# Kernel optimization log

Measured on AMD Instinct MI355X. Metric: run time of the kernel, lower is better.

## Reference

```python
import jax, jax.numpy as jnp
import numpy as np

H = 128          # hidden_channels == num_features for both node types
L = 3            # num_layers
E_TYPES = 3      # (a->a), (a->b), (b->a)
N = 200000       # nodes per type
E = 600000       # edges per edge type
G = 64           # graphs in batch
C = 10           # num_classes
BN_EPS = 1e-5


def setup_inputs() -> dict:
    key = jax.random.key(0)
    ks = jax.random.split(key, 16)
    x_a = jax.random.normal(ks[0], (N, H), dtype=jnp.float32)
    x_b = jax.random.normal(ks[1], (N, H), dtype=jnp.float32)
    ei_aa = jax.random.randint(ks[2], (2, E), 0, N, dtype=jnp.int32)
    ei_ab = jax.random.randint(ks[3], (2, E), 0, N, dtype=jnp.int32)
    ei_ba = jax.random.randint(ks[4], (2, E), 0, N, dtype=jnp.int32)
    batch_a = jnp.sort(jax.random.randint(ks[5], (N,), 0, G, dtype=jnp.int32))
    batch_b = jnp.sort(jax.random.randint(ks[6], (N,), 0, G, dtype=jnp.int32))
    s = 1.0 / np.sqrt(H)
    # GraphConv params per (layer, edge_type): lin_rel (weight+bias), lin_root (no bias)
    Wrel = jax.random.uniform(ks[7], (L, E_TYPES, H, H), jnp.float32, -s, s)
    brel = jax.random.uniform(ks[8], (L, E_TYPES, H), jnp.float32, -s, s)
    Wroot = jax.random.uniform(ks[9], (L, E_TYPES, H, H), jnp.float32, -s, s)
    # BatchNorm affine params per node type (0='a', 1='b')
    bn_gamma = jnp.ones((2, H), jnp.float32)
    bn_beta = jnp.zeros((2, H), jnp.float32)
    lin_W = jax.random.uniform(ks[10], (C, H), jnp.float32, -s, s)
    lin_b = jax.random.uniform(ks[11], (C,), jnp.float32, -s, s)
    return {"x_a": x_a, "x_b": x_b, "Wrel": Wrel, "brel": brel, "Wroot": Wroot,
            "bn_gamma": bn_gamma, "bn_beta": bn_beta, "lin_W": lin_W, "lin_b": lin_b,
            "ei_aa": ei_aa, "ei_ab": ei_ab, "ei_ba": ei_ba,
            "batch_a": batch_a, "batch_b": batch_b}


def _graph_conv(x_src, x_dst, ei, W_rel, b_rel, W_root):
    # PyG GraphConv (aggr='add'): out = lin_rel(sum_{j in N(i)} x_j) + lin_root(x_i)
    agg = jax.ops.segment_sum(x_src[ei[0]], ei[1], num_segments=x_dst.shape[0])
    return agg @ W_rel.T + b_rel + x_dst @ W_root.T


def _bn(x, gamma, beta):
    # BatchNorm in training mode: batch statistics (biased variance)
    mu = x.mean(axis=0)
    var = x.var(axis=0)
    return gamma * (x - mu) * jax.lax.rsqrt(var + BN_EPS) + beta


def reference(x_a, x_b, Wrel, brel, Wroot, bn_gamma, bn_beta, lin_W, lin_b,
              ei_aa, ei_ab, ei_ba, batch_a, batch_b):
    for l in range(L):
        # HeteroConv sums contributions per destination node type
        out_a = (_graph_conv(x_a, x_a, ei_aa, Wrel[l, 0], brel[l, 0], Wroot[l, 0]) +
                 _graph_conv(x_b, x_a, ei_ba, Wrel[l, 2], brel[l, 2], Wroot[l, 2]))
        out_b = _graph_conv(x_a, x_b, ei_ab, Wrel[l, 1], brel[l, 1], Wroot[l, 1])
        x_a = _bn(jax.nn.relu(out_a), bn_gamma[0], bn_beta[0])
        x_b = _bn(jax.nn.relu(out_b), bn_gamma[1], bn_beta[1])
    # global mean pool over concatenated node types
    feats = jnp.concatenate([x_a, x_b], axis=0)
    batch = jnp.concatenate([batch_a, batch_b], axis=0)
    sums = jax.ops.segment_sum(feats, batch, num_segments=G)
    counts = jax.ops.segment_sum(jnp.ones((feats.shape[0],), feats.dtype), batch, num_segments=G)
    pooled = sums / jnp.maximum(counts, 1.0)[:, None]
    return pooled @ lin_W.T + lin_b
```

## Files before the change

### kernel.cpp

```cpp
#include <hip/hip_runtime.h>
#include <hip/hip_bf16.h>

#define HF 128

typedef unsigned int uint32;
typedef unsigned short ushort16;
typedef float f32x4 __attribute__((ext_vector_type(4)));
typedef __bf16 bf16x8 __attribute__((ext_vector_type(8)));

__device__ __forceinline__ float bflo(uint32 u) { return __uint_as_float(u << 16); }
__device__ __forceinline__ float bfhi(uint32 u) { return __uint_as_float(u & 0xffff0000u); }
__device__ __forceinline__ ushort16 f2bf(float f) {
  uint32 u = __float_as_uint(f);
  return (ushort16)((u + 0x7fffu + ((u >> 16) & 1u)) >> 16);
}
__device__ __forceinline__ uint32 pack2(float lo, float hi) {
  return (uint32)f2bf(lo) | ((uint32)f2bf(hi) << 16);
}

__global__ void diag_k(float* __restrict__ out, int n, float val) {
  int i = blockIdx.x * 256 + threadIdx.x;
  if (i < n) out[i] = val;
}

__global__ void init_k(float* __restrict__ ss, float* __restrict__ pool, int Gn) {
  int idx = blockIdx.x * 256 + threadIdx.x;
  if (idx < 512) ss[idx] = (idx < 128 || (idx >= 256 && idx < 384)) ? 1.f : 0.f;
  int p = idx - 512;
  if (p >= 0 && p < Gn * HF) pool[p] = 0.f;
}

__global__ void conv_k(const float* __restrict__ in, uint32* __restrict__ out, int n4) {
  int i = blockIdx.x * 256 + threadIdx.x;
  if (i >= n4) return;
  float4 v = ((const float4*)in)[i];
  uint2 p;
  p.x = pack2(v.x, v.y);
  p.y = pack2(v.z, v.w);
  ((uint2*)out)[i] = p;
}

__global__ void count_k(const int* __restrict__ ei, int E, int* __restrict__ rp) {
  int e = blockIdx.x * 256 + threadIdx.x;
  if (e < E) atomicAdd(&rp[ei[E + e]], 1);
}

__global__ __launch_bounds__(256) void scan1_k(const int* __restrict__ rp, int N,
                                               int* __restrict__ bsum) {
  int b = blockIdx.x, t = threadIdx.x;
  int i = b * 1024 + t * 4;
  int s = 0;
  if (i + 3 < N) {
    int4 v = *(const int4*)&rp[i];
    s = v.x + v.y + v.z + v.w;
  } else {
    for (int j = 0; j < 4; ++j) if (i + j < N) s += rp[i + j];
  }
  __shared__ int sd[256];
  sd[t] = s;
  __syncthreads();
  for (int o = 128; o > 0; o >>= 1) {
    if (t < o) sd[t] += sd[t + o];
    __syncthreads();
  }
  if (t == 0) bsum[b] = sd[0];
}

__global__ __launch_bounds__(1024) void scan2_k(int* __restrict__ bsum, int nb) {
  __shared__ int sd[1024];
  int t = threadIdx.x;
  int v = (t < nb) ? bsum[t] : 0;
  sd[t] = v;
  __syncthreads();
  for (int o = 1; o < 1024; o <<= 1) {
    int x = (t >= o) ? sd[t - o] : 0;
    __syncthreads();
    sd[t] += x;
    __syncthreads();
  }
  if (t < nb) bsum[t] = sd[t] - v;
}

__global__ __launch_bounds__(256) void scan3_k(int* __restrict__ rp, int* __restrict__ cur,
                                               const int* __restrict__ bsum, int N) {
  int b = blockIdx.x, t = threadIdx.x;
  int i = b * 1024 + t * 4;
  int c[4];
  #pragma unroll
  for (int j = 0; j < 4; ++j) c[j] = (i + j < N) ? rp[i + j] : 0;
  int tsum = c[0] + c[1] + c[2] + c[3];
  __shared__ int sd[256];
  sd[t] = tsum;
  __syncthreads();
  for (int o = 1; o < 256; o <<= 1) {
    int x = (t >= o) ? sd[t - o] : 0;
    __syncthreads();
    sd[t] += x;
    __syncthreads();
  }
  int off = bsum[b] + sd[t] - tsum;
  int p = off;
  #pragma unroll
  for (int j = 0; j < 4; ++j) {
    if (i + j < N) { rp[i + j] = p; cur[i + j] = p; }
    p += c[j];
  }
  if (i < N && N <= i + 4) rp[N] = off + tsum;
}

__global__ void fill_k(const int* __restrict__ ei, int E, int* __restrict__ cur,
                       int* __restrict__ cs) {
  int e = blockIdx.x * 256 + threadIdx.x;
  if (e >= E) return;
  int dst = ei[E + e];
  int pos = atomicAdd(&cur[dst], 1);
  cs[pos] = ei[e];
}

__global__ __launch_bounds__(128) void prep2_k(
    const float* __restrict__ Wrel_l, const float* __restrict__ Wroot_l,
    const float* __restrict__ brel_l, const float* __restrict__ ss,
    ushort16* __restrict__ BWa, ushort16* __restrict__ BWb,
    float* __restrict__ uvec) {
  __shared__ float red[128];
  int n = blockIdx.x, k = threadIdx.x;
  float scA = ss[k], shA = ss[128 + k], scB = ss[256 + k], shB = ss[384 + k];
  float w0  = Wrel_l[n * HF + k];
  float w1  = Wrel_l[16384 + n * HF + k];
  float w2  = Wrel_l[32768 + n * HF + k];
  float wr1 = Wroot_l[16384 + n * HF + k];
  float wrc = Wroot_l[n * HF + k] + Wroot_l[32768 + n * HF + k];

  int ksl = k >> 5;
  int lane = (n & 15) + (((k >> 3) & 3) << 4);
  int j = k & 7;
  int nt = n >> 4;
  auto put = [&](ushort16* B, int ksb, float v) {
    B[((size_t)((ksb + ksl) * 8 + nt) * 64 + lane) * 8 + j] = f2bf(v);
  };
  put(BWa, 0, scA * w0);
  put(BWa, 4, scB * w2);
  put(BWa, 8, scA * wrc);
  put(BWb, 0, scA * w1);
  put(BWb, 4, scB * wr1);

  auto reduce = [&](float v) -> float {
    red[k] = v;
    __syncthreads();
    for (int s = 64; s > 0; s >>= 1) {
      if (k < s) red[k] += red[k + s];
      __syncthreads();
    }
    float r = red[0];
    __syncthreads();
    return r;
  };
  float r0 = reduce(shA * w0);
  float r1 = reduce(shB * w2);
  float r2 = reduce(shA * w1);
  float r3 = reduce(shA * wrc);
  float r4 = reduce(shB * wr1);
  if (k == 0) {
    uvec[n]       = r0;
    uvec[128 + n] = r1;
    uvec[256 + n] = r2;
    uvec[384 + n] = brel_l[n] + brel_l[256 + n] + r3;
    uvec[512 + n] = brel_l[128 + n] + r4;
  }
}

template <bool HAS2>
__global__ __launch_bounds__(256) void gg_k(
    const uint32* __restrict__ Xg1, const int* __restrict__ rp1, const int* __restrict__ cs1,
    const uint32* __restrict__ Xg2, const int* __restrict__ rp2, const int* __restrict__ cs2,
    const uint32* Xr,
    const bf16x8* __restrict__ BW,
    const float* __restrict__ u1, const float* __restrict__ u2,
    const float* __restrict__ bias,
    uint32* out,
    float* __restrict__ statS, float* __restrict__ statQ,
    int nRows) {
  constexpr int KS_G = HAS2 ? 8 : 4;
  constexpr int WDW = HAS2 ? 2048 : 1088;
  __shared__ uint32 lds[4][WDW];
  int tid = threadIdx.x, wid = tid >> 6, l = tid & 63;
  int R0 = blockIdx.x * 64 + wid * 16;
  uint32* L = &lds[wid][0];
  int grp = l >> 4, sub = l & 15;
  int row = l & 15, khi = l >> 4;

  int grr = R0 + row;
  bf16x8 rt[4];
  #pragma unroll
  for (int ks = 0; ks < 4; ++ks) {
    rt[ks] = bf16x8{};
    if (grr < nRows)
      rt[ks] = *(const bf16x8*)&Xr[(size_t)grr * 64 + ks * 16 + khi * 4];
  }

  #pragma unroll
  for (int rr = 0; rr < 4; ++rr) {
    int r = rr * 4 + grp;
    int gr = R0 + r;
    int dstOff = r * 64 + ((sub ^ (r & 7)) << 2);
    {
      float a0=0.f,a1=0.f,a2=0.f,a3=0.f,a4=0.f,a5=0.f,a6=0.f,a7=0.f;
      if (gr < nRows) {
        int e0 = rp1[gr], e1 = rp1[gr + 1];
        int e = e0;
        for (; e + 2 <= e1; e += 2) {
          int s0 = cs1[e], s1 = cs1[e + 1];
          uint4 v0 = *(const uint4*)&Xg1[(size_t)s0 * 64 + sub * 4];
          uint4 v1 = *(const uint4*)&Xg1[(size_t)s1 * 64 + sub * 4];
          a0 += bflo(v0.x) + bflo(v1.x); a1 += bfhi(v0.x) + bfhi(v1.x);
          a2 += bflo(v0.y) + bflo(v1.y); a3 += bfhi(v0.y) + bfhi(v1.y);
          a4 += bflo(v0.z) + bflo(v1.z); a5 += bfhi(v0.z) + bfhi(v1.z);
          a6 += bflo(v0.w) + bflo(v1.w); a7 += bfhi(v0.w) + bfhi(v1.w);
        }
        if (e < e1) {
          uint4 v = *(const uint4*)&Xg1[(size_t)cs1[e] * 64 + sub * 4];
          a0 += bflo(v.x); a1 += bfhi(v.x); a2 += bflo(v.y); a3 += bfhi(v.y);
          a4 += bflo(v.z); a5 += bfhi(v.z); a6 += bflo(v.w); a7 += bfhi(v.w);
        }
      }
      uint4 p;
      p.x = pack2(a0, a1); p.y = pack2(a2, a3);
      p.z = pack2(a4, a5); p.w = pack2(a6, a7);
      *(uint4*)&L[dstOff] = p;
    }
    if constexpr (HAS2) {
      float a0=0.f,a1=0.f,a2=0.f,a3=0.f,a4=0.f,a5=0.f,a6=0.f,a7=0.f;
      if (gr < nRows) {
        int e0 = rp2[gr], e1 = rp2[gr + 1];
        int e = e0;
        for (; e + 2 <= e1; e += 2) {
          int s0 = cs2[e], s1 = cs2[e + 1];
          uint4 v0 = *(const uint4*)&Xg2[(size_t)s0 * 64 + sub * 4];
          uint4 v1 = *(const uint4*)&Xg2[(size_t)s1 * 64 + sub * 4];
          a0 += bflo(v0.x) + bflo(v1.x); a1 += bfhi(v0.x) + bfhi(v1.x);
          a2 += bflo(v0.y) + bflo(v1.y); a3 += bfhi(v0.y) + bfhi(v1.y);
          a4 += bflo(v0.z) + bflo(v1.z); a5 += bfhi(v0.z) + bfhi(v1.z);
          a6 += bflo(v0.w) + bflo(v1.w); a7 += bfhi(v0.w) + bfhi(v1.w);
        }
        if (e < e1) {
          uint4 v = *(const uint4*)&Xg2[(size_t)cs2[e] * 64 + sub * 4];
          a0 += bflo(v.x); a1 += bfhi(v.x); a2 += bflo(v.y); a3 += bfhi(v.y);
          a4 += bflo(v.z); a5 += bfhi(v.z); a6 += bflo(v.w); a7 += bfhi(v.w);
        }
      }
      uint4 p;
      p.x = pack2(a0, a1); p.y = pack2(a2, a3);
      p.z = pack2(a4, a5); p.w = pack2(a6, a7);
      *(uint4*)&L[1024 + dstOff] = p;
    }
  }

  f32x4 acc[8] = {};
  #pragma unroll
  for (int ks = 0; ks < 4; ++ks) {
    int d = row * 64 + (((ks * 4 + khi) ^ (row & 7)) << 2);
    bf16x8 a = *(const bf16x8*)&L[d];
    const bf16x8* Bp = BW + (size_t)(ks * 8) * 64 + l;
    #pragma unroll
    for (int nt = 0; nt < 8; ++nt) {
      bf16x8 b = Bp[(size_t)nt * 64];
      acc[nt] = __builtin_amdgcn_mfma_f32_16x16x32_bf16(a, b, acc[nt], 0, 0, 0);
    }
  }
  if constexpr (HAS2) {
    #pragma unroll
    for (int ks = 0; ks < 4; ++ks) {
      int d = 1024 + row * 64 + (((ks * 4 + khi) ^ (row & 7)) << 2);
      bf16x8 a = *(const bf16x8*)&L[d];
      const bf16x8* Bp = BW + (size_t)((4 + ks) * 8) * 64 + l;
      #pragma unroll
      for (int nt = 0; nt < 8; ++nt) {
        bf16x8 b = Bp[(size_t)nt * 64];
        acc[nt] = __builtin_amdgcn_mfma_f32_16x16x32_bf16(a, b, acc[nt], 0, 0, 0);
      }
    }
  }
  #pragma unroll
  for (int ks = 0; ks < 4; ++ks) {
    const bf16x8* Bp = BW + (size_t)((KS_G + ks) * 8) * 64 + l;
    #pragma unroll
    for (int nt = 0; nt < 8; ++nt) {
      bf16x8 b = Bp[(size_t)nt * 64];
      acc[nt] = __builtin_amdgcn_mfma_f32_16x16x32_bf16(rt[ks], b, acc[nt], 0, 0, 0);
    }
  }

  int rl0 = khi * 4;
  float deg1v[4], deg2v[4];
  #pragma unroll
  for (int j = 0; j < 4; ++j) {
    int r = R0 + rl0 + j;
    deg1v[j] = (r < nRows) ? (float)(rp1[r + 1] - rp1[r]) : 0.f;
    if constexpr (HAS2) deg2v[j] = (r < nRows) ? (float)(rp2[r + 1] - rp2[r]) : 0.f;
    else deg2v[j] = 0.f;
  }
  ushort16* P = (ushort16*)L;
  int c0 = l & 15;
  float ps[8], pq[8];
  #pragma unroll
  for (int nt = 0; nt < 8; ++nt) {
    int col = nt * 16 + c0;
    float bc = bias[col];
    float u1c = u1[col];
    float u2c = HAS2 ? u2[col] : 0.f;
    float s = 0.f, q = 0.f;
    #pragma unroll
    for (int j = 0; j < 4; ++j) {
      float v = acc[nt][j] + bc + deg1v[j] * u1c;
      if constexpr (HAS2) v += deg2v[j] * u2c;
      v = fmaxf(v, 0.f);
      if (R0 + rl0 + j < nRows) { s += v; q += v * v; }
      P[(rl0 + j) * 136 + col] = f2bf(v);
    }
    ps[nt] = s; pq[nt] = q;
  }

  #pragma unroll
  for (int rr = 0; rr < 4; ++rr) {
    int rloc = rr * 4 + khi;
    int grow = R0 + rloc;
    if (grow < nRows) {
      uint4 v = *(const uint4*)&P[rloc * 136 + c0 * 8];
      *(uint4*)&out[(size_t)grow * 64 + c0 * 4] = v;
    }
  }

  #pragma unroll
  for (int nt = 0; nt < 8; ++nt) {
    ps[nt] += __shfl_xor(ps[nt], 16); ps[nt] += __shfl_xor(ps[nt], 32);
    pq[nt] += __shfl_xor(pq[nt], 16); pq[nt] += __shfl_xor(pq[nt], 32);
  }
  if (l < 16) {
    float* S = statS + (size_t)(blockIdx.x & 63) * 128;
    float* Q = statQ + (size_t)(blockIdx.x & 63) * 128;
    #pragma unroll
    for (int nt = 0; nt < 8; ++nt) {
      unsafeAtomicAdd(&S[nt * 16 + l], ps[nt]);
      unsafeAtomicAdd(&Q[nt * 16 + l], pq[nt]);
    }
  }
}

__global__ void bn_fin_k(const float* __restrict__ stats, const float* __restrict__ gamma,
                         const float* __restrict__ beta, float* __restrict__ ss,
                         float nA, float nB) {
  int t = threadIdx.x;
  if (t >= 256) return;
  int type = t >> 7, f = t & 127;
  const float* S = stats + (size_t)type * 16384;
  const float* Q = S + 8192;
  float s = 0.f, q = 0.f;
  for (int st = 0; st < 64; ++st) { s += S[st * 128 + f]; q += Q[st * 128 + f]; }
  float nN = type ? nB : nA;
  float mean = s / nN;
  float var = q / nN - mean * mean;
  float rstd = rsqrtf(var + 1e-5f);
  float sc = gamma[type * HF + f] * rstd;
  float sh = beta[type * HF + f] - mean * sc;
  ss[type * 256 + f] = sc;
  ss[type * 256 + 128 + f] = sh;
}

__global__ __launch_bounds__(256) void pool_k(const uint32* __restrict__ x,
                                              const int* __restrict__ batch,
                                              const float* __restrict__ scale,
                                              const float* __restrict__ shift,
                                              float* __restrict__ pool, int nN) {
  int f2 = threadIdx.x & 31;
  int sub = threadIdx.x >> 5;
  int start = blockIdx.x * 1024;
  int end = min(start + 1024, nN);
  float4 sc = *(const float4*)&scale[f2 * 4];
  float4 sh = *(const float4*)&shift[f2 * 4];
  float a0 = 0.f, a1 = 0.f, a2 = 0.f, a3 = 0.f, cnt = 0.f;
  int cur = -1;
  for (int n = start + sub; n < end; n += 8) {
    int g = batch[n];
    if (g != cur) {
      if (cur >= 0) {
        float* bp = &pool[(size_t)cur * HF + f2 * 4];
        unsafeAtomicAdd(bp + 0, sc.x * a0 + cnt * sh.x);
        unsafeAtomicAdd(bp + 1, sc.y * a1 + cnt * sh.y);
        unsafeAtomicAdd(bp + 2, sc.z * a2 + cnt * sh.z);
        unsafeAtomicAdd(bp + 3, sc.w * a3 + cnt * sh.w);
      }
      a0 = a1 = a2 = a3 = 0.f; cnt = 0.f; cur = g;
    }
    uint2 v = *(const uint2*)&x[(size_t)n * 64 + f2 * 2];
    a0 += bflo(v.x); a1 += bfhi(v.x); a2 += bflo(v.y); a3 += bfhi(v.y);
    cnt += 1.f;
  }
  if (cur >= 0) {
    float* bp = &pool[(size_t)cur * HF + f2 * 4];
    unsafeAtomicAdd(bp + 0, sc.x * a0 + cnt * sh.x);
    unsafeAtomicAdd(bp + 1, sc.y * a1 + cnt * sh.y);
    unsafeAtomicAdd(bp + 2, sc.z * a2 + cnt * sh.z);
    unsafeAtomicAdd(bp + 3, sc.w * a3 + cnt * sh.w);
  }
}

__device__ inline int lowerb(const int* a, int n, int v) {
  int lo = 0, hi = n;
  while (lo < hi) { int m = (lo + hi) >> 1; if (a[m] < v) lo = m + 1; else hi = m; }
  return lo;
}

__global__ void counts_k(const int* __restrict__ ba, int nA, const int* __restrict__ bb, int nB,
                         float* __restrict__ counts, int Gn) {
  for (int g = threadIdx.x; g < Gn; g += blockDim.x) {
    int c = (lowerb(ba, nA, g + 1) - lowerb(ba, nA, g)) +
            (lowerb(bb, nB, g + 1) - lowerb(bb, nB, g));
    counts[g] = fmaxf((float)c, 1.f);
  }
}

__global__ void final_k(const float* __restrict__ pool, const float* __restrict__ counts,
                        const float* __restrict__ linW, const float* __restrict__ linb,
                        float* __restrict__ out, int Cn) {
  int g = blockIdx.x;
  int lane = threadIdx.x;
  float inv = 1.f / counts[g];
  float p0 = pool[(size_t)g * HF + lane] * inv;
  float p1 = pool[(size_t)g * HF + 64 + lane] * inv;
  for (int c = 0; c < Cn; ++c) {
    float t = p0 * linW[c * HF + lane] + p1 * linW[c * HF + 64 + lane];
    for (int off = 32; off > 0; off >>= 1) t += __shfl_down(t, off);
    if (lane == 0) out[g * Cn + c] = t + linb[c];
  }
}

extern "C" void kernel_launch(void* const* d_in, const int* in_sizes, int n_in,
                              void* d_out, int out_size, void* d_ws, size_t ws_size,
                              hipStream_t stream) {
  const float* x_a   = (const float*)d_in[0];
  const float* x_b   = (const float*)d_in[1];
  const float* Wrel  = (const float*)d_in[2];
  const float* brel  = (const float*)d_in[3];
  const float* Wroot = (const float*)d_in[4];
  const float* bn_g  = (const float*)d_in[5];
  const float* bn_b  = (const float*)d_in[6];
  const float* lin_W = (const float*)d_in[7];
  const float* lin_b = (const float*)d_in[8];
  const int* ei_aa   = (const int*)d_in[9];
  const int* ei_ab   = (const int*)d_in[10];
  const int* ei_ba   = (const int*)d_in[11];
  const int* batch_a = (const int*)d_in[12];
  const int* batch_b = (const int*)d_in[13];

  int Na  = in_sizes[0] / HF;
  int Nb  = in_sizes[1] / HF;
  int Eaa = in_sizes[9] / 2;
  int Eab = in_sizes[10] / 2;
  int Eba = in_sizes[11] / 2;
  int Cn  = in_sizes[7] / HF;
  int Gn  = out_size / Cn;

  size_t NHa = (size_t)Na * HF, NHb = (size_t)Nb * HF;
  char* base = (char*)d_ws;
  auto alignup = [](size_t x) { return (x + 255) & ~(size_t)255; };
  size_t off = 0;
  size_t oXA0 = off; off = alignup(off + NHa * 2);
  size_t oXA1 = off; off = alignup(off + NHa * 2);
  size_t oXB  = off; off = alignup(off + NHb * 2);
  size_t oRP  = off; off = alignup(off + ((size_t)(Na + 1) + (Nb + 1) + (Na + 1)) * 4);
  size_t oCUR = off; off = alignup(off + ((size_t)Na + Nb + Na) * 4);
  size_t oCS  = off; off = alignup(off + ((size_t)Eaa + Eab + Eba) * 4);
  size_t oBWA = off; off = alignup(off + (size_t)12 * 8 * 64 * 16);
  size_t oBWB = off; off = alignup(off + (size_t)8 * 8 * 64 * 16);
  size_t oUV  = off; off = alignup(off + 5 * 128 * 4);
  size_t oSS  = off; off = alignup(off + 512 * 4);
  size_t oST  = off; off = alignup(off + 32768 * 4);
  size_t oBS  = off; off = alignup(off + 1024 * 4);
  size_t oPOOL= off; off = alignup(off + (size_t)Gn * HF * 4);
  size_t oCNT = off; off = alignup(off + (size_t)Gn * 4);
  size_t need = off;

  if (ws_size < need) {
    diag_k<<<(out_size + 255) / 256, 256, 0, stream>>>(
        (float*)d_out, out_size, (float)((double)ws_size / 1048576.0));
    return;
  }

  uint32* XA0 = (uint32*)(base + oXA0);
  uint32* XA1 = (uint32*)(base + oXA1);
  uint32* XB  = (uint32*)(base + oXB);
  int* rp_aa = (int*)(base + oRP);
  int* rp_ab = rp_aa + (Na + 1);
  int* rp_ba = rp_ab + (Nb + 1);
  int* cur_aa = (int*)(base + oCUR);
  int* cur_ab = cur_aa + Na;
  int* cur_ba = cur_ab + Nb;
  int* cs_aa = (int*)(base + oCS);
  int* cs_ab = cs_aa + Eaa;
  int* cs_ba = cs_ab + Eab;
  ushort16* BWa = (ushort16*)(base + oBWA);
  ushort16* BWb = (ushort16*)(base + oBWB);
  float* uvec  = (float*)(base + oUV);
  float* ss    = (float*)(base + oSS);
  float* stats = (float*)(base + oST);
  int* bsum    = (int*)(base + oBS);
  float* pool  = (float*)(base + oPOOL);
  float* counts= (float*)(base + oCNT);

  float* ss_a = ss;
  float* ss_b = ss + 256;
  float* uaa = uvec, *uba = uvec + 128, *uab = uvec + 256;
  float* bias_a = uvec + 384, *bias_b = uvec + 512;
  float* SA = stats, *QA = stats + 8192, *SB = stats + 16384, *QB = stats + 24576;

  init_k<<<(512 + Gn * HF + 255) / 256, 256, 0, stream>>>(ss, pool, Gn);
  conv_k<<<((int)(NHa / 4) + 255) / 256, 256, 0, stream>>>(x_a, XA0, (int)(NHa / 4));
  conv_k<<<((int)(NHb / 4) + 255) / 256, 256, 0, stream>>>(x_b, XB, (int)(NHb / 4));

  hipMemsetAsync(rp_aa, 0, ((size_t)(Na + 1) + (Nb + 1) + (Na + 1)) * 4, stream);
  count_k<<<(Eaa + 255) / 256, 256, 0, stream>>>(ei_aa, Eaa, rp_aa);
  count_k<<<(Eab + 255) / 256, 256, 0, stream>>>(ei_ab, Eab, rp_ab);
  count_k<<<(Eba + 255) / 256, 256, 0, stream>>>(ei_ba, Eba, rp_ba);

  int nb_a = (Na + 1023) / 1024;
  int nb_b = (Nb + 1023) / 1024;
  scan1_k<<<nb_a, 256, 0, stream>>>(rp_aa, Na, bsum);
  scan2_k<<<1, 1024, 0, stream>>>(bsum, nb_a);
  scan3_k<<<nb_a, 256, 0, stream>>>(rp_aa, cur_aa, bsum, Na);
  scan1_k<<<nb_b, 256, 0, stream>>>(rp_ab, Nb, bsum);
  scan2_k<<<1, 1024, 0, stream>>>(bsum, nb_b);
  scan3_k<<<nb_b, 256, 0, stream>>>(rp_ab, cur_ab, bsum, Nb);
  scan1_k<<<nb_a, 256, 0, stream>>>(rp_ba, Na, bsum);
  scan2_k<<<1, 1024, 0, stream>>>(bsum, nb_a);
  scan3_k<<<nb_a, 256, 0, stream>>>(rp_ba, cur_ba, bsum, Na);

  fill_k<<<(Eaa + 255) / 256, 256, 0, stream>>>(ei_aa, Eaa, cur_aa, cs_aa);
  fill_k<<<(Eab + 255) / 256, 256, 0, stream>>>(ei_ab, Eab, cur_ab, cs_ab);
  fill_k<<<(Eba + 255) / 256, 256, 0, stream>>>(ei_ba, Eba, cur_ba, cs_ba);

  uint32* xa_cur = XA0;
  uint32* xa_nxt = XA1;
  for (int l = 0; l < 3; ++l) {
    const float* Wrel_l  = Wrel  + (size_t)l * 3 * 16384;
    const float* Wroot_l = Wroot + (size_t)l * 3 * 16384;
    const float* brel_l  = brel  + (size_t)l * 3 * HF;

    prep2_k<<<128, 128, 0, stream>>>(Wrel_l, Wroot_l, brel_l, ss, BWa, BWb, uvec);
    hipMemsetAsync(stats, 0, 32768 * 4, stream);

    gg_k<true><<<(Na + 63) / 64, 256, 0, stream>>>(
        xa_cur, rp_aa, cs_aa, XB, rp_ba, cs_ba, xa_cur,
        (const bf16x8*)BWa, uaa, uba, bias_a, xa_nxt, SA, QA, Na);
    gg_k<false><<<(Nb + 63) / 64, 256, 0, stream>>>(
        xa_cur, rp_ab, cs_ab, nullptr, nullptr, nullptr, XB,
        (const bf16x8*)BWb, uab, nullptr, bias_b, XB, SB, QB, Nb);

    bn_fin_k<<<1, 256, 0, stream>>>(stats, bn_g, bn_b, ss, (float)Na, (float)Nb);

    uint32* t = xa_cur; xa_cur = xa_nxt; xa_nxt = t;
  }

  pool_k<<<(Na + 1023) / 1024, 256, 0, stream>>>(xa_cur, batch_a, ss_a, ss_a + 128, pool, Na);
  pool_k<<<(Nb + 1023) / 1024, 256, 0, stream>>>(XB, batch_b, ss_b, ss_b + 128, pool, Nb);
  counts_k<<<1, 256, 0, stream>>>(batch_a, Na, batch_b, Nb, counts, Gn);
  final_k<<<Gn, 64, 0, stream>>>(pool, counts, lin_W, lin_b, (float*)d_out, Cn);
}
```

Measured before the change: 1.147 ms.

## Batch CSR build launches across edge types and unroll the neighbor gather by four

Merges the three per-edge-type count, scan and fill kernels into single launches that dispatch on block index, with separate block-sum buffers per edge type. Folds the stats memset into the weight-prep kernel. Rewrites the gather loop to issue up to four neighbor loads per iteration, reading the column indices past the row end; the column array is padded so those reads stay in bounds. The aim is fewer launches and more memory parallelism in the gather, at the cost of extra index loads and branches.

Result: slower. 1.200 ms (+4.6%).

```diff
diff --git a/kernel.cpp b/kernel.cpp
--- a/kernel.cpp
+++ b/kernel.cpp
@@ -40,14 +40,21 @@
   ((uint2*)out)[i] = p;
 }
 
-__global__ void count_k(const int* __restrict__ ei, int E, int* __restrict__ rp) {
-  int e = blockIdx.x * 256 + threadIdx.x;
+__global__ void count3_k(const int* __restrict__ eA, int EA, int* __restrict__ rA,
+                         const int* __restrict__ eB, int EB, int* __restrict__ rB,
+                         const int* __restrict__ eC, int EC, int* __restrict__ rC,
+                         int B0, int B1) {
+  int b = blockIdx.x;
+  const int* ei; int E; int* rp;
+  if (b < B0)            { ei = eA; E = EA; rp = rA; }
+  else if (b < B0 + B1)  { ei = eB; E = EB; rp = rB; b -= B0; }
+  else                   { ei = eC; E = EC; rp = rC; b -= B0 + B1; }
+  int e = b * 256 + threadIdx.x;
   if (e < E) atomicAdd(&rp[ei[E + e]], 1);
 }
 
-__global__ __launch_bounds__(256) void scan1_k(const int* __restrict__ rp, int N,
-                                               int* __restrict__ bsum) {
-  int b = blockIdx.x, t = threadIdx.x;
+__device__ __forceinline__ void scan1_body(const int* __restrict__ rp, int N,
+                                           int* __restrict__ bsum, int b, int t) {
   int i = b * 1024 + t * 4;
   int s = 0;
   if (i + 3 < N) {
@@ -66,7 +73,21 @@
   if (t == 0) bsum[b] = sd[0];
 }
 
-__global__ __launch_bounds__(1024) void scan2_k(int* __restrict__ bsum, int nb) {
+__global__ __launch_bounds__(256) void scan1x3_k(
+    const int* __restrict__ rA, int NA, int* __restrict__ bA,
+    const int* __restrict__ rB, int NB, int* __restrict__ bB,
+    const int* __restrict__ rC, int NC, int* __restrict__ bC, int nbA, int nbB) {
+  int b = blockIdx.x;
+  if (b < nbA)            scan1_body(rA, NA, bA, b, threadIdx.x);
+  else if (b < nbA + nbB) scan1_body(rB, NB, bB, b - nbA, threadIdx.x);
+  else                    scan1_body(rC, NC, bC, b - nbA - nbB, threadIdx.x);
+}
+
+__global__ __launch_bounds__(1024) void scan2x3_k(int* __restrict__ bA, int nbA,
+                                                  int* __restrict__ bB, int nbB,
+                                                  int* __restrict__ bC, int nbC) {
+  int* bsum = (blockIdx.x == 0) ? bA : (blockIdx.x == 1) ? bB : bC;
+  int nb    = (blockIdx.x == 0) ? nbA : (blockIdx.x == 1) ? nbB : nbC;
   __shared__ int sd[1024];
   int t = threadIdx.x;
   int v = (t < nb) ? bsum[t] : 0;
@@ -81,9 +102,9 @@
   if (t < nb) bsum[t] = sd[t] - v;
 }
 
-__global__ __launch_bounds__(256) void scan3_k(int* __restrict__ rp, int* __restrict__ cur,
-                                               const int* __restrict__ bsum, int N) {
-  int b = blockIdx.x, t = threadIdx.x;
+__device__ __forceinline__ void scan3_body(int* __restrict__ rp, int* __restrict__ cur,
+                                           const int* __restrict__ bsum, int N,
+                                           int b, int t) {
   int i = b * 1024 + t * 4;
   int c[4];
   #pragma unroll
@@ -108,9 +129,27 @@
   if (i < N && N <= i + 4) rp[N] = off + tsum;
 }
 
-__global__ void fill_k(const int* __restrict__ ei, int E, int* __restrict__ cur,
-                       int* __restrict__ cs) {
-  int e = blockIdx.x * 256 + threadIdx.x;
+__global__ __launch_bounds__(256) void scan3x3_k(
+    int* __restrict__ rA, int* __restrict__ cA, const int* __restrict__ bA, int NA,
+    int* __restrict__ rB, int* __restrict__ cB, const int* __restrict__ bB, int NB,
+    int* __restrict__ rC, int* __restrict__ cC, const int* __restrict__ bC, int NC,
+    int nbA, int nbB) {
+  int b = blockIdx.x;
+  if (b < nbA)            scan3_body(rA, cA, bA, NA, b, threadIdx.x);
+  else if (b < nbA + nbB) scan3_body(rB, cB, bB, NB, b - nbA, threadIdx.x);
+  else                    scan3_body(rC, cC, bC, NC, b - nbA - nbB, threadIdx.x);
+}
+
+__global__ void fill3_k(const int* __restrict__ eA, int EA, int* __restrict__ cuA, int* __restrict__ csA,
+                        const int* __restrict__ eB, int EB, int* __restrict__ cuB, int* __restrict__ csB,
+                        const int* __restrict__ eC, int EC, int* __restrict__ cuC, int* __restrict__ csC,
+                        int B0, int B1) {
+  int b = blockIdx.x;
+  const int* ei; int E; int* cur; int* cs;
+  if (b < B0)           { ei = eA; E = EA; cur = cuA; cs = csA; }
+  else if (b < B0 + B1) { ei = eB; E = EB; cur = cuB; cs = csB; b -= B0; }
+  else                  { ei = eC; E = EC; cur = cuC; cs = csC; b -= B0 + B1; }
+  int e = b * 256 + threadIdx.x;
   if (e >= E) return;
   int dst = ei[E + e];
   int pos = atomicAdd(&cur[dst], 1);
@@ -121,9 +160,13 @@
     const float* __restrict__ Wrel_l, const float* __restrict__ Wroot_l,
     const float* __restrict__ brel_l, const float* __restrict__ ss,
     ushort16* __restrict__ BWa, ushort16* __restrict__ BWb,
-    float* __restrict__ uvec) {
+    float* __restrict__ uvec, float* __restrict__ stats) {
   __shared__ float red[128];
   int n = blockIdx.x, k = threadIdx.x;
+  if (n < 64) {
+    float4 z = make_float4(0.f, 0.f, 0.f, 0.f);
+    *(float4*)&stats[n * 512 + k * 4] = z;
+  }
   float scA = ss[k], shA = ss[128 + k], scB = ss[256 + k], shB = ss[384 + k];
   float w0  = Wrel_l[n * HF + k];
   float w1  = Wrel_l[16384 + n * HF + k];
@@ -198,62 +241,58 @@
       rt[ks] = *(const bf16x8*)&Xr[(size_t)grr * 64 + ks * 16 + khi * 4];
   }
 
-  #pragma unroll
-  for (int rr = 0; rr < 4; ++rr) {
-    int r = rr * 4 + grp;
-    int gr = R0 + r;
-    int dstOff = r * 64 + ((sub ^ (r & 7)) << 2);
-    {
-      float a0=0.f,a1=0.f,a2=0.f,a3=0.f,a4=0.f,a5=0.f,a6=0.f,a7=0.f;
+  auto gather_tile = [&](const uint32* __restrict__ Xg, const int* __restrict__ rp,
+                         const int* __restrict__ cs, int ldsBase) {
+    #pragma unroll
+    for (int rr = 0; rr < 4; ++rr) {
+      int r = rr * 4 + grp;
+      int gr = R0 + r;
+      float lo0 = 0.f, lo1 = 0.f, lo2 = 0.f, lo3 = 0.f;
+      float hi0 = 0.f, hi1 = 0.f, hi2 = 0.f, hi3 = 0.f;
       if (gr < nRows) {
-        int e0 = rp1[gr], e1 = rp1[gr + 1];
-        int e = e0;
-        for (; e + 2 <= e1; e += 2) {
-          int s0 = cs1[e], s1 = cs1[e + 1];
-          uint4 v0 = *(const uint4*)&Xg1[(size_t)s0 * 64 + sub * 4];
-          uint4 v1 = *(const uint4*)&Xg1[(size_t)s1 * 64 + sub * 4];
-          a0 += bflo(v0.x) + bflo(v1.x); a1 += bfhi(v0.x) + bfhi(v1.x);
-          a2 += bflo(v0.y) + bflo(v1.y); a3 += bfhi(v0.y) + bfhi(v1.y);
-          a4 += bflo(v0.z) + bflo(v1.z); a5 += bfhi(v0.z) + bfhi(v1.z);
-          a6 += bflo(v0.w) + bflo(v1.w); a7 += bfhi(v0.w) + bfhi(v1.w);
-        }
-        if (e < e1) {
-          uint4 v = *(const uint4*)&Xg1[(size_t)cs1[e] * 64 + sub * 4];
-          a0 += bflo(v.x); a1 += bfhi(v.x); a2 += bflo(v.y); a3 += bfhi(v.y);
-          a4 += bflo(v.z); a5 += bfhi(v.z); a6 += bflo(v.w); a7 += bfhi(v.w);
+        int e0 = rp[gr], e1 = rp[gr + 1];
+        for (int e = e0; e < e1; e += 4) {
+          int rem = e1 - e;
+          int i0 = cs[e], i1 = cs[e + 1], i2 = cs[e + 2], i3 = cs[e + 3];
+          {
+            uint4 v = *(const uint4*)&Xg[(size_t)i0 * 64 + sub * 4];
+            hi0 += __uint_as_float(v.x); lo0 += __uint_as_float(v.x << 16);
+            hi1 += __uint_as_float(v.y); lo1 += __uint_as_float(v.y << 16);
+            hi2 += __uint_as_float(v.z); lo2 += __uint_as_float(v.z << 16);
+            hi3 += __uint_as_float(v.w); lo3 += __uint_as_float(v.w << 16);
+          }
+          if (rem > 1) {
+            uint4 v = *(const uint4*)&Xg[(size_t)i1 * 64 + sub * 4];
+            hi0 += __uint_as_float(v.x); lo0 += __uint_as_float(v.x << 16);
+            hi1 += __uint_as_float(v.y); lo1 += __uint_as_float(v.y << 16);
+            hi2 += __uint_as_float(v.z); lo2 += __uint_as_float(v.z << 16);
+            hi3 += __uint_as_float(v.w); lo3 += __uint_as_float(v.w << 16);
+          }
+          if (rem > 2) {
+            uint4 v = *(const uint4*)&Xg[(size_t)i2 * 64 + sub * 4];
+            hi0 += __uint_as_float(v.x); lo0 += __uint_as_float(v.x << 16);
+            hi1 += __uint_as_float(v.y); lo1 += __uint_as_float(v.y << 16);
+            hi2 += __uint_as_float(v.z); lo2 += __uint_as_float(v.z << 16);
+            hi3 += __uint_as_float(v.w); lo3 += __uint_as_float(v.w << 16);
+          }
+          if (rem > 3) {
+            uint4 v = *(const uint4*)&Xg[(size_t)i3 * 64 + sub * 4];
+            hi0 += __uint_as_float(v.x); lo0 += __uint_as_float(v.x << 16);
+            hi1 += __uint_as_float(v.y); lo1 += __uint_as_float(v.y << 16);
+            hi2 += __uint_as_float(v.z); lo2 += __uint_as_float(v.z << 16);
+            hi3 += __uint_as_float(v.w); lo3 += __uint_as_float(v.w << 16);
+          }
         }
       }
       uint4 p;
-      p.x = pack2(a0, a1); p.y = pack2(a2, a3);
-      p.z = pack2(a4, a5); p.w = pack2(a6, a7);
-      *(uint4*)&L[dstOff] = p;
-    }
-    if constexpr (HAS2) {
-      float a0=0.f,a1=0.f,a2=0.f,a3=0.f,a4=0.f,a5=0.f,a6=0.f,a7=0.f;
-      if (gr < nRows) {
-        int e0 = rp2[gr], e1 = rp2[gr + 1];
-        int e = e0;
-        for (; e + 2 <= e1; e += 2) {
-          int s0 = cs2[e], s1 = cs2[e + 1];
-          uint4 v0 = *(const uint4*)&Xg2[(size_t)s0 * 64 + sub * 4];
-          uint4 v1 = *(const uint4*)&Xg2[(size_t)s1 * 64 + sub * 4];
-          a0 += bflo(v0.x) + bflo(v1.x); a1 += bfhi(v0.x) + bfhi(v1.x);
-          a2 += bflo(v0.y) + bflo(v1.y); a3 += bfhi(v0.y) + bfhi(v1.y);
-          a4 += bflo(v0.z) + bflo(v1.z); a5 += bfhi(v0.z) + bfhi(v1.z);
-          a6 += bflo(v0.w) + bflo(v1.w); a7 += bfhi(v0.w) + bfhi(v1.w);
-        }
-        if (e < e1) {
-          uint4 v = *(const uint4*)&Xg2[(size_t)cs2[e] * 64 + sub * 4];
-          a0 += bflo(v.x); a1 += bfhi(v.x); a2 += bflo(v.y); a3 += bfhi(v.y);
-          a4 += bflo(v.z); a5 += bfhi(v.z); a6 += bflo(v.w); a7 += bfhi(v.w);
-        }
-      }
-      uint4 p;
-      p.x = pack2(a0, a1); p.y = pack2(a2, a3);
-      p.z = pack2(a4, a5); p.w = pack2(a6, a7);
-      *(uint4*)&L[1024 + dstOff] = p;
-    }
-  }
+      p.x = pack2(lo0, hi0); p.y = pack2(lo1, hi1);
+      p.z = pack2(lo2, hi2); p.w = pack2(lo3, hi3);
+      *(uint4*)&L[ldsBase + r * 64 + ((sub ^ (r & 7)) << 2)] = p;
+    }
+  };
+
+  gather_tile(Xg1, rp1, cs1, 0);
+  if constexpr (HAS2) gather_tile(Xg2, rp2, cs2, 1024);
 
   f32x4 acc[8] = {};
   #pragma unroll
@@ -469,13 +508,13 @@
   size_t oXB  = off; off = alignup(off + NHb * 2);
   size_t oRP  = off; off = alignup(off + ((size_t)(Na + 1) + (Nb + 1) + (Na + 1)) * 4);
   size_t oCUR = off; off = alignup(off + ((size_t)Na + Nb + Na) * 4);
-  size_t oCS  = off; off = alignup(off + ((size_t)Eaa + Eab + Eba) * 4);
+  size_t oCS  = off; off = alignup(off + ((size_t)Eaa + Eab + Eba + 16) * 4);
   size_t oBWA = off; off = alignup(off + (size_t)12 * 8 * 64 * 16);
   size_t oBWB = off; off = alignup(off + (size_t)8 * 8 * 64 * 16);
   size_t oUV  = off; off = alignup(off + 5 * 128 * 4);
   size_t oSS  = off; off = alignup(off + 512 * 4);
   size_t oST  = off; off = alignup(off + 32768 * 4);
-  size_t oBS  = off; off = alignup(off + 1024 * 4);
+  size_t oBS  = off; off = alignup(off + 3072 * 4);
   size_t oPOOL= off; off = alignup(off + (size_t)Gn * HF * 4);
   size_t oCNT = off; off = alignup(off + (size_t)Gn * 4);
   size_t need = off;
@@ -518,25 +557,22 @@
   conv_k<<<((int)(NHb / 4) + 255) / 256, 256, 0, stream>>>(x_b, XB, (int)(NHb / 4));
 
   hipMemsetAsync(rp_aa, 0, ((size_t)(Na + 1) + (Nb + 1) + (Na + 1)) * 4, stream);
-  count_k<<<(Eaa + 255) / 256, 256, 0, stream>>>(ei_aa, Eaa, rp_aa);
-  count_k<<<(Eab + 255) / 256, 256, 0, stream>>>(ei_ab, Eab, rp_ab);
-  count_k<<<(Eba + 255) / 256, 256, 0, stream>>>(ei_ba, Eba, rp_ba);
+  int B0 = (Eaa + 255) / 256, B1 = (Eab + 255) / 256, B2 = (Eba + 255) / 256;
+  count3_k<<<B0 + B1 + B2, 256, 0, stream>>>(ei_aa, Eaa, rp_aa, ei_ab, Eab, rp_ab,
+                                             ei_ba, Eba, rp_ba, B0, B1);
 
   int nb_a = (Na + 1023) / 1024;
   int nb_b = (Nb + 1023) / 1024;
-  scan1_k<<<nb_a, 256, 0, stream>>>(rp_aa, Na, bsum);
-  scan2_k<<<1, 1024, 0, stream>>>(bsum, nb_a);
-  scan3_k<<<nb_a, 256, 0, stream>>>(rp_aa, cur_aa, bsum, Na);
-  scan1_k<<<nb_b, 256, 0, stream>>>(rp_ab, Nb, bsum);
-  scan2_k<<<1, 1024, 0, stream>>>(bsum, nb_b);
-  scan3_k<<<nb_b, 256, 0, stream>>>(rp_ab, cur_ab, bsum, Nb);
-  scan1_k<<<nb_a, 256, 0, stream>>>(rp_ba, Na, bsum);
-  scan2_k<<<1, 1024, 0, stream>>>(bsum, nb_a);
-  scan3_k<<<nb_a, 256, 0, stream>>>(rp_ba, cur_ba, bsum, Na);
-
-  fill_k<<<(Eaa + 255) / 256, 256, 0, stream>>>(ei_aa, Eaa, cur_aa, cs_aa);
-  fill_k<<<(Eab + 255) / 256, 256, 0, stream>>>(ei_ab, Eab, cur_ab, cs_ab);
-  fill_k<<<(Eba + 255) / 256, 256, 0, stream>>>(ei_ba, Eba, cur_ba, cs_ba);
+  scan1x3_k<<<nb_a + nb_b + nb_a, 256, 0, stream>>>(
+      rp_aa, Na, bsum, rp_ab, Nb, bsum + 1024, rp_ba, Na, bsum + 2048, nb_a, nb_b);
+  scan2x3_k<<<3, 1024, 0, stream>>>(bsum, nb_a, bsum + 1024, nb_b, bsum + 2048, nb_a);
+  scan3x3_k<<<nb_a + nb_b + nb_a, 256, 0, stream>>>(
+      rp_aa, cur_aa, bsum, Na, rp_ab, cur_ab, bsum + 1024, Nb,
+      rp_ba, cur_ba, bsum + 2048, Na, nb_a, nb_b);
+
+  fill3_k<<<B0 + B1 + B2, 256, 0, stream>>>(ei_aa, Eaa, cur_aa, cs_aa,
+                                            ei_ab, Eab, cur_ab, cs_ab,
+                                            ei_ba, Eba, cur_ba, cs_ba, B0, B1);
 
   uint32* xa_cur = XA0;
   uint32* xa_nxt = XA1;
@@ -545,8 +581,7 @@
     const float* Wroot_l = Wroot + (size_t)l * 3 * 16384;
     const float* brel_l  = brel  + (size_t)l * 3 * HF;
 
-    prep2_k<<<128, 128, 0, stream>>>(Wrel_l, Wroot_l, brel_l, ss, BWa, BWb, uvec);
-    hipMemsetAsync(stats, 0, 32768 * 4, stream);
+    prep2_k<<<128, 128, 0, stream>>>(Wrel_l, Wroot_l, brel_l, ss, BWa, BWb, uvec, stats);
 
     gg_k<true><<<(Na + 63) / 64, 256, 0, stream>>>(
         xa_cur, rp_aa, cs_aa, XB, rp_ba, cs_ba, xa_cur,
```
